# Performance work log

Measured on AMD Instinct MI355X. Metric: run time of the kernel, lower is better.

## Reference

```python
import jax, jax.numpy as jnp
import numpy as np

T, B, H, OUT = 64, 4096, 256, 2
SLOPE = 25.0  # snntorch surrogate.fast_sigmoid default slope


@jax.custom_vjp
def spike(x):
    # Heaviside forward, fast-sigmoid surrogate gradient backward
    return (x > 0).astype(x.dtype)

def _spk_fwd(x):
    return (x > 0).astype(x.dtype), x

def _spk_bwd(x, g):
    return (g / (SLOPE * jnp.abs(x) + 1.0) ** 2,)

spike.defvjp(_spk_fwd, _spk_bwd)


def temporal_embedding(length):
    center = length // 2
    sigma = length / 10
    pos = np.arange(length)
    e = np.exp(-0.5 * ((pos - center) / sigma) ** 2)
    e = (e - e.min()) / (e.max() - e.min())
    return jnp.asarray(e, dtype=jnp.float32)


def setup_inputs() -> dict:
    key = jax.random.key(0)
    ks = jax.random.split(key, 16)

    def lin(k, o, i):
        bound = 1.0 / np.sqrt(i)
        kw, kb = jax.random.split(k)
        W = jax.random.uniform(kw, (o, i), minval=-bound, maxval=bound, dtype=jnp.float32)
        b = jax.random.uniform(kb, (o,), minval=-bound, maxval=bound, dtype=jnp.float32)
        return W, b

    W_in, b_in = lin(ks[0], H, 3)
    W_h, b_h = lin(ks[1], H, H)
    W_h2, b_h2 = lin(ks[2], H, H)
    W_out, b_out = lin(ks[3], OUT, H)
    W_pred, b_pred = lin(ks[4], OUT, T * 4)
    u = lambda k, n: jax.random.uniform(k, (n,), dtype=jnp.float32)
    return {
        "x": jax.random.normal(ks[5], (T, B, 3), dtype=jnp.float32),
        "W_in": W_in, "b_in": b_in,
        "beta_in": u(ks[6], H), "thr_in": u(ks[7], H),
        "W_h": W_h, "b_h": b_h,
        "beta_h": u(ks[8], H), "thr_h": u(ks[9], H),
        "W_h2": W_h2, "b_h2": b_h2,
        "beta_h2": u(ks[10], H), "thr_h2": u(ks[11], H),
        "W_out": W_out, "b_out": b_out,
        "beta_out": u(ks[12], OUT),
        "W_pred": W_pred, "b_pred": b_pred,
    }


def reference(x, W_in, b_in, beta_in, thr_in, W_h, b_h, beta_h, thr_h,
              W_h2, b_h2, beta_h2, thr_h2, W_out, b_out, beta_out,
              W_pred, b_pred):
    Tn, Bsz = x.shape[0], x.shape[1]
    emb = temporal_embedding(Tn)
    x = x * emb[:, None, None]  # per-timestep Gaussian temporal weighting

    def lif(cur, mem, beta, thr):
        # snnTorch Leaky, reset_mechanism='subtract': reset from PREVIOUS mem (detached)
        reset = jax.lax.stop_gradient((mem - thr > 0).astype(cur.dtype))
        mem = jnp.clip(beta, 0.0, 1.0) * mem + cur - reset * thr
        return spike(mem - thr), mem

    def step(carry, x_t):
        m1, m2, m4, m3 = carry
        s1, m1 = lif(x_t @ W_in.T + b_in, m1, beta_in, thr_in)
        s2, m2 = lif(s1 @ W_h.T + b_h, m2, beta_h, thr_h)
        s4, m4 = lif(s2 @ W_h2.T + b_h2, m4, beta_h2, thr_h2)
        # li_out: reset_mechanism='none', default threshold=1.0
        m3 = jnp.clip(beta_out, 0.0, 1.0) * m3 + s4 @ W_out.T + b_out
        spk_out = spike(m3 - 1.0)
        return (m1, m2, m4, m3), (spk_out, m3)

    z = lambda n: jnp.zeros((Bsz, n), x.dtype)
    init = (z(W_in.shape[0]), z(W_h.shape[0]), z(W_h2.shape[0]), z(W_out.shape[0]))
    _, (spk_rec, mem_rec) = jax.lax.scan(step, init, x)
    out = jnp.concatenate([spk_rec, mem_rec], axis=-1)  # [T, B, 2*OUT]
    # torch .view(B, T*2*OUT) on contiguous [T,B,2*OUT] == plain reshape
    out = out.reshape(Bsz, Tn * out.shape[-1])
    return out @ W_pred.T + b_pred  # [B, OUT]
```

## Files before the change

kernel.cpp:

```cpp
#include <hip/hip_runtime.h>
#include <hip/hip_bf16.h>

#define TT 64
#define BB 4096
#define HH 256
#define BMb 16
#define NBLK (BB / BMb)
#define TC 4
#define NCH (TT / TC)

typedef short bf16x8_t __attribute__((ext_vector_type(8)));
typedef float f32x4_t  __attribute__((ext_vector_type(4)));

#define WS_WA_B   0u
#define WS_EMB_B  786432u
#define WS_REC_B  1048576u

__device__ __forceinline__ float clip01f(float v) {
    return fminf(fmaxf(v, 0.0f), 1.0f);
}

__global__ __launch_bounds__(64) void setup_emb_kernel(float* __restrict__ emb) {
    int i = threadIdx.x;
    const double sigma = 64.0 / 10.0;
    const double c = 32.0;
    double d = ((double)i - c) / sigma;
    double e = exp(-0.5 * (d * d));
    double d0 = (0.0 - c) / sigma;
    double emin = exp(-0.5 * (d0 * d0));
    emb[i] = (float)((e - emin) / (1.0 - emin));
}

__global__ __launch_bounds__(256) void split_weights_kernel(
    const float* __restrict__ W_h, const float* __restrict__ W_h2,
    unsigned short* __restrict__ WA)
{
    int flat = blockIdx.x * 256 + threadIdx.x;
    int j     = flat & 7;
    int lane  = (flat >> 3) & 63;
    int ntile = (flat >> 9) & 15;
    int kt    = (flat >> 13) & 7;
    int rest  = flat >> 16;
    int part  = rest % 3;
    int layer = rest / 3;
    int k = kt * 32 + (lane >> 4) * 8 + j;
    int n = ntile * 16 + (lane & 15);
    const float* W = layer ? W_h2 : W_h;
    float w = W[n * HH + k];
    __hip_bfloat16 h = __float2bfloat16(w);
    float r1 = w - __bfloat162float(h);
    __hip_bfloat16 m = __float2bfloat16(r1);
    float r2 = r1 - __bfloat162float(m);
    __hip_bfloat16 l = __float2bfloat16(r2);
    __hip_bfloat16 v = (part == 0) ? h : ((part == 1) ? m : l);
    WA[flat] = *reinterpret_cast<unsigned short*>(&v);
}

union U16x8 { uint4 u; bf16x8_t v; };


#define AS1 __attribute__((address_space(1)))
#define AS3 __attribute__((address_space(3)))
__device__ __forceinline__ void gl16(const void* g, void* l) {
    __builtin_amdgcn_global_load_lds((AS1 const void*)g, (AS3 void*)l, 16, 0, 0);
}

#define ISSUE6(Wc, ktn, sl) do {                                               \
    const char* gb_ = (const char*)(Wc) + (ktn) * 16384;                       \
    char* lb_ = myring + (sl) * 6144;                                          \
    gl16(gb_,          lb_);                                                   \
    gl16(gb_ + 1024,   lb_ + 1024);                                            \
    gl16(gb_ + 131072, lb_ + 2048);                                            \
    gl16(gb_ + 132096, lb_ + 3072);                                            \
    gl16(gb_ + 262144, lb_ + 4096);                                            \
    gl16(gb_ + 263168, lb_ + 5120);                                            \
} while (0)

#define MFMA8T(wa_, wb_, ktb) do {                                             \
    _Pragma("unroll")                                                          \
    for (int tt_ = 0; tt_ < TC; ++tt_) {                                       \
        U16x8 br_; br_.u = BfL[tt_ * 512 + (ktb) * 64];                        \
        D0[tt_] = __builtin_amdgcn_mfma_f32_16x16x32_bf16(wa_.v, br_.v, D0[tt_], 0, 0, 0); \
        D1[tt_] = __builtin_amdgcn_mfma_f32_16x16x32_bf16(wb_.v, br_.v, D1[tt_], 0, 0, 0); \
    }                                                                          \
} while (0)

#define STEPT(sl, ktb, Wi, kti) do {                                           \
    asm volatile("s_waitcnt vmcnt(6)" ::: "memory");                           \
    __builtin_amdgcn_sched_barrier(0);                                         \
    {                                                                          \
        U16x8 wa_, wb_;                                                        \
        wa_.u = ringRd[(sl) * 384 + 0];                                        \
        wb_.u = ringRd[(sl) * 384 + 64];                                       \
        asm volatile("s_waitcnt lgkmcnt(0)" ::: "memory");                     \
        __builtin_amdgcn_sched_barrier(0);                                     \
        MFMA8T(wa_, wb_, ktb);                                                 \
    }                                                                          \
    {                                                                          \
        U16x8 wa_, wb_;                                                        \
        wa_.u = ringRd[(sl) * 384 + 128];                                      \
        wb_.u = ringRd[(sl) * 384 + 192];                                      \
        asm volatile("s_waitcnt lgkmcnt(0)" ::: "memory");                     \
        __builtin_amdgcn_sched_barrier(0);                                     \
        MFMA8T(wa_, wb_, ktb);                                                 \
    }                                                                          \
    {                                                                          \
        U16x8 wa_, wb_;                                                        \
        wa_.u = ringRd[(sl) * 384 + 256];                                      \
        wb_.u = ringRd[(sl) * 384 + 320];                                      \
        asm volatile("s_waitcnt lgkmcnt(0)" ::: "memory");                     \
        __builtin_amdgcn_sched_barrier(0);                                     \
        ISSUE6(Wi, kti, sl);                                                   \
        __builtin_amdgcn_sched_barrier(0);                                     \
        MFMA8T(wa_, wb_, ktb);                                                 \
    }                                                                          \
} while (0)

#define GPHASE(Wc, Wn) do {                                                    \
    STEPT(0, 0, Wc, 2);                                                        \
    STEPT(1, 1, Wc, 3);                                                        \
    STEPT(0, 2, Wc, 4);                                                        \
    STEPT(1, 3, Wc, 5);                                                        \
    STEPT(0, 4, Wc, 6);                                                        \
    STEPT(1, 5, Wc, 7);                                                        \
    STEPT(0, 6, Wn, 0);                                                        \
    STEPT(1, 7, Wn, 1);                                                        \
} while (0)

__device__ __forceinline__ void compute_p(
    const float* __restrict__ WoutS, const unsigned long long (*__restrict__ M3Lt)[4],
    int wb, int ooc, float* __restrict__ pout, int lane)
{
    if (lane < 32) {
        float p = 0.f;
        for (int k = 0; k < HH; ++k) {
            int ww = k >> 4, gg = (k >> 2) & 3, reg = k & 3;
            unsigned long long word = M3Lt[ww][reg];
            unsigned w32 = (gg < 2) ? (unsigned)word : (unsigned)(word >> 32);
            int sh = ((gg & 1) << 4) | wb;
            unsigned bit = (w32 >> sh) & 1u;
            float wv = WoutS[ooc * HH + k];
            p = p + (bit ? wv : 0.f);
        }
        pout[lane] = p;
    }
}

__device__ __forceinline__ void li_walker_bits(
    const float* __restrict__ WoutS, const unsigned long long (*__restrict__ M3Lt)[4],
    int wb, int ooc, float bto, float bo, float& m3s,
    float* __restrict__ rec, int t, int b0, int lane)
{
    if (lane < 32) {
        float p = 0.f;
        for (int k = 0; k < HH; ++k) {
            int ww = k >> 4, gg = (k >> 2) & 3, reg = k & 3;
            unsigned long long word = M3Lt[ww][reg];
            unsigned w32 = (gg < 2) ? (unsigned)word : (unsigned)(word >> 32);
            int sh = ((gg & 1) << 4) | wb;
            unsigned bit = (w32 >> sh) & 1u;
            float wv = WoutS[ooc * HH + k];
            p = p + (bit ? wv : 0.f);
        }
        float mm3 = fmaf(bto, m3s, p);
        mm3 = mm3 + bo;
        m3s = mm3;
        float spk = ((m3s - 1.0f) > 0.f) ? 1.f : 0.f;
        float om3 = __shfl_xor(m3s, 16, 64);
        float osp = __shfl_xor(spk, 16, 64);
        if (lane < 16) {
            *(float4*)(rec + ((size_t)t * BB + b0 + wb) * 4) =
                make_float4(spk, osp, m3s, om3);
        }
    }
}

__global__ __launch_bounds__(512) void snn_main_kernel(
    const float* __restrict__ x,
    const float* __restrict__ W_in, const float* __restrict__ b_in,
    const float* __restrict__ beta_in, const float* __restrict__ thr_in,
    const float* __restrict__ b_h, const float* __restrict__ beta_h, const float* __restrict__ thr_h,
    const float* __restrict__ b_h2, const float* __restrict__ beta_h2, const float* __restrict__ thr_h2,
    const float* __restrict__ W_out, const float* __restrict__ b_out, const float* __restrict__ beta_out,
    const unsigned short* __restrict__ WA, const float* __restrict__ emb,
    float* __restrict__ rec)
{
#pragma clang fp contract(off)
    const int tid = threadIdx.x;
    const int w = tid >> 6;
    const int lane = tid & 63;
    const int b = lane & 15;
    const int g = lane >> 4;
    const int b0 = blockIdx.x * BMb;

    __shared__ __align__(16) unsigned short frag[TC][8 * 64 * 8];
    __shared__ unsigned long long M3L[TC][16][4];
    __shared__ float pbuf[TC][32];
    __shared__ __align__(16) float WoutS[2 * HH];
    __shared__ float4 PL1a[HH];
    __shared__ float2 PL1b[HH];
    __shared__ float4 PL2[HH];
    __shared__ float4 PL3[HH];
    __shared__ float  xs[TT][BMb][3];
    __shared__ float  embS[TT];
    __shared__ __align__(16) char ring[8 * 2 * 6144];

    char* myring = ring + w * 12288;
    const uint4* ringRd = (const uint4*)(ring + w * 12288 + lane * 16);
    const uint4* BfL = (const uint4*)frag + lane;

    WoutS[tid] = W_out[tid];
    if (tid < HH) {
        int n = tid;
        PL1a[n] = make_float4(W_in[n * 3], W_in[n * 3 + 1], W_in[n * 3 + 2], b_in[n]);
        PL1b[n] = make_float2(clip01f(beta_in[n]), thr_in[n]);
        PL2[n]  = make_float4(b_h[n],  clip01f(beta_h[n]),  thr_h[n],  0.f);
        PL3[n]  = make_float4(b_h2[n], clip01f(beta_h2[n]), thr_h2[n], 0.f);
    }
    if (tid < TT) embS[tid] = emb[tid];
#pragma unroll
    for (int i = tid; i < TT * BMb; i += 512) {
        int ts = i >> 4, bb = i & 15;
        const float* xp = x + ((size_t)ts * BB + b0 + bb) * 3;
        xs[ts][bb][0] = xp[0];
        xs[ts][bb][1] = xp[1];
        xs[ts][bb][2] = xp[2];
    }

    const int nb0 = w * 32 + g * 4;

    float m1[2][4], m2[2][4], m4[2][4];
#pragma unroll
    for (int u = 0; u < 2; ++u)
#pragma unroll
        for (int r = 0; r < 4; ++r) { m1[u][r] = 0.f; m2[u][r] = 0.f; m4[u][r] = 0.f; }

    const int sb0 = ((w * 64 + ((g >> 1) * 16 + b)) * 8 + (g & 1) * 4);

    const int wb = lane & 15;
    const int ooc = (lane >> 4) & 1;
    float bto = clip01f(beta_out[ooc]);
    float bo = b_out[ooc];
    float m3s = 0.f;

    const uint4* W2 = (const uint4*)WA + (size_t)(2 * w) * 64 + lane;
    const uint4* W3 = W2 + 24576;

    ISSUE6(W2, 0, 0);
    ISSUE6(W2, 1, 1);

    __syncthreads();

#pragma unroll 1
    for (int c = 0; c < NCH; ++c) {
        const int t0 = c * TC;

#pragma unroll
        for (int tt = 0; tt < TC; ++tt) {
            const int t = t0 + tt;
            float et = embS[t];
            float xe0 = xs[t][b][0] * et;
            float xe1 = xs[t][b][1] * et;
            float xe2 = xs[t][b][2] * et;
            unsigned sp[2][4];
#pragma unroll
            for (int u = 0; u < 2; ++u)
#pragma unroll
            for (int r = 0; r < 4; ++r) {
                int n = nb0 + u * 16 + r;
                float4 pa = PL1a[n];
                float2 pb = PL1b[n];
                float a1 = xe0 * pa.x;
                a1 = fmaf(xe1, pa.y, a1);
                a1 = fmaf(xe2, pa.z, a1);
                float cur = a1 + pa.w;
                float rf = ((m1[u][r] - pb.y) > 0.f) ? 1.f : 0.f;
                float mm = fmaf(pb.x, m1[u][r], cur);
                mm = fmaf(-rf, pb.y, mm);
                m1[u][r] = mm;
                sp[u][r] = ((mm - pb.y) > 0.f) ? 0x3F80u : 0u;
            }
            *(uint2*)(&frag[tt][sb0])       = make_uint2(sp[0][0] | (sp[0][1] << 16), sp[0][2] | (sp[0][3] << 16));
            *(uint2*)(&frag[tt][sb0 + 256]) = make_uint2(sp[1][0] | (sp[1][1] << 16), sp[1][2] | (sp[1][3] << 16));
        }
        __syncthreads();

        if (w < TC && c > 0)
            compute_p(WoutS, M3L[w], wb, ooc, pbuf[w], lane);

        f32x4_t D0[TC], D1[TC];
#pragma unroll
        for (int tt = 0; tt < TC; ++tt) {
            D0[tt] = (f32x4_t){0.f, 0.f, 0.f, 0.f};
            D1[tt] = (f32x4_t){0.f, 0.f, 0.f, 0.f};
        }
        GPHASE(W2, W3);

        uint2 s2w[TC][2];
#pragma unroll
        for (int tt = 0; tt < TC; ++tt) {
            unsigned sp[2][4];
#pragma unroll
            for (int r = 0; r < 4; ++r) {
                int n0 = nb0 + r;
                float4 p2 = PL2[n0];
                float cur = D0[tt][r] + p2.x;
                float rf = ((m2[0][r] - p2.z) > 0.f) ? 1.f : 0.f;
                float mm = fmaf(p2.y, m2[0][r], cur);
                mm = fmaf(-rf, p2.z, mm);
                m2[0][r] = mm;
                sp[0][r] = ((mm - p2.z) > 0.f) ? 0x3F80u : 0u;
            }
#pragma unroll
            for (int r = 0; r < 4; ++r) {
                int n1 = nb0 + 16 + r;
                float4 p2 = PL2[n1];
                float cur = D1[tt][r] + p2.x;
                float rf = ((m2[1][r] - p2.z) > 0.f) ? 1.f : 0.f;
                float mm = fmaf(p2.y, m2[1][r], cur);
                mm = fmaf(-rf, p2.z, mm);
                m2[1][r] = mm;
                sp[1][r] = ((mm - p2.z) > 0.f) ? 0x3F80u : 0u;
            }
            s2w[tt][0] = make_uint2(sp[0][0] | (sp[0][1] << 16), sp[0][2] | (sp[0][3] << 16));
            s2w[tt][1] = make_uint2(sp[1][0] | (sp[1][1] << 16), sp[1][2] | (sp[1][3] << 16));
        }
        __syncthreads();

        if (w == 0 && c > 0 && lane < 32) {
#pragma unroll
            for (int tt = 0; tt < TC; ++tt) {
                float p = pbuf[tt][lane];
                float mm3 = fmaf(bto, m3s, p);
                mm3 = mm3 + bo;
                m3s = mm3;
                float spk = ((m3s - 1.0f) > 0.f) ? 1.f : 0.f;
                float om3 = __shfl_xor(m3s, 16, 64);
                float osp = __shfl_xor(spk, 16, 64);
                if (lane < 16) {
                    *(float4*)(rec + ((size_t)(t0 - TC + tt) * BB + b0 + wb) * 4) =
                        make_float4(spk, osp, m3s, om3);
                }
            }
        }

#pragma unroll
        for (int tt = 0; tt < TC; ++tt) {
            *(uint2*)(&frag[tt][sb0])       = s2w[tt][0];
            *(uint2*)(&frag[tt][sb0 + 256]) = s2w[tt][1];
        }
        __syncthreads();

#pragma unroll
        for (int tt = 0; tt < TC; ++tt) {
            D0[tt] = (f32x4_t){0.f, 0.f, 0.f, 0.f};
            D1[tt] = (f32x4_t){0.f, 0.f, 0.f, 0.f};
        }
        GPHASE(W3, W2);

#pragma unroll
        for (int tt = 0; tt < TC; ++tt) {
#pragma unroll
            for (int u = 0; u < 2; ++u) {
#pragma unroll
                for (int r = 0; r < 4; ++r) {
                    int n = nb0 + u * 16 + r;
                    float4 p3 = PL3[n];
                    float cur = ((u == 0) ? D0[tt][r] : D1[tt][r]) + p3.x;
                    float rf = ((m4[u][r] - p3.z) > 0.f) ? 1.f : 0.f;
                    float mm = fmaf(p3.y, m4[u][r], cur);
                    mm = fmaf(-rf, p3.z, mm);
                    m4[u][r] = mm;
                    bool s3 = (mm - p3.z) > 0.f;
                    unsigned long long mk = __ballot(s3);
                    if (lane == 0) M3L[tt][2 * w + u][r] = mk;
                }
            }
        }
        __syncthreads();
    }

    if (w == 0) {
#pragma unroll
        for (int tt = 0; tt < TC; ++tt)
            li_walker_bits(WoutS, M3L[tt], wb, ooc, bto, bo, m3s,
                           rec, TT - TC + tt, b0, lane);
    }
}

__global__ __launch_bounds__(256) void pred_kernel(
    const float* __restrict__ rec, const float* __restrict__ W_pred,
    const float* __restrict__ b_pred, float* __restrict__ out)
{
#pragma clang fp contract(off)
    int r = blockIdx.x * 256 + threadIdx.x;
    const float* f = rec + (size_t)r * 256;
    float a0 = 0.f, a1 = 0.f;
#pragma unroll 4
    for (int c = 0; c < 256; ++c) {
        float v = f[c];
        a0 = fmaf(v, W_pred[c], a0);
        a1 = fmaf(v, W_pred[256 + c], a1);
    }
    out[r * 2 + 0] = a0 + b_pred[0];
    out[r * 2 + 1] = a1 + b_pred[1];
}

extern "C" void kernel_launch(void* const* d_in, const int* in_sizes, int n_in,
                              void* d_out, int out_size, void* d_ws, size_t ws_size,
                              hipStream_t stream)
{
    const float* x        = (const float*)d_in[0];
    const float* W_in     = (const float*)d_in[1];
    const float* b_in     = (const float*)d_in[2];
    const float* beta_in  = (const float*)d_in[3];
    const float* thr_in   = (const float*)d_in[4];
    const float* W_h      = (const float*)d_in[5];
    const float* b_h      = (const float*)d_in[6];
    const float* beta_h   = (const float*)d_in[7];
    const float* thr_h    = (const float*)d_in[8];
    const float* W_h2     = (const float*)d_in[9];
    const float* b_h2     = (const float*)d_in[10];
    const float* beta_h2  = (const float*)d_in[11];
    const float* thr_h2   = (const float*)d_in[12];
    const float* W_out    = (const float*)d_in[13];
    const float* b_out    = (const float*)d_in[14];
    const float* beta_out = (const float*)d_in[15];
    const float* W_pred   = (const float*)d_in[16];
    const float* b_pred   = (const float*)d_in[17];

    char* ws = (char*)d_ws;
    unsigned short* WA = (unsigned short*)(ws + WS_WA_B);
    float* emb = (float*)(ws + WS_EMB_B);
    float* rec = (float*)(ws + WS_REC_B);

    split_weights_kernel<<<1536, 256, 0, stream>>>(W_h, W_h2, WA);
    setup_emb_kernel<<<1, 64, 0, stream>>>(emb);

    snn_main_kernel<<<NBLK, 512, 0, stream>>>(
        x, W_in, b_in, beta_in, thr_in,
        b_h, beta_h, thr_h,
        b_h2, beta_h2, thr_h2,
        W_out, b_out, beta_out,
        WA, emb, rec);

    pred_kernel<<<BB / 256, 256, 0, stream>>>(rec, W_pred, b_pred, (float*)d_out);
}
```

Before: 668.3 us.

## Halve main kernel to 4 waves each computing 64 output neurons

The main SNN kernel now runs 256 threads (4 waves) instead of 512. Each wave owns 64 hidden neurons instead of 32, so every B fragment loaded from LDS feeds four MFMAs instead of two, and the per-wave weight ring doubles to 12 async loads per stage. The aim is fewer waves contending for LDS and barriers, with more reuse of the spike fragments per wave. The cost is higher register pressure (16 accumulators per timestep chunk, larger membrane arrays) and less latency hiding per block, which may lower occupancy.

```diff
diff --git a/kernel.cpp b/kernel.cpp
--- a/kernel.cpp
+++ b/kernel.cpp
@@ -65,54 +65,68 @@
     __builtin_amdgcn_global_load_lds((AS1 const void*)g, (AS3 void*)l, 16, 0, 0);
 }
 
-#define ISSUE6(Wc, ktn, sl) do {                                               \
+#define ISSUE12(Wc, ktn, sl) do {                                              \
     const char* gb_ = (const char*)(Wc) + (ktn) * 16384;                       \
-    char* lb_ = myring + (sl) * 6144;                                          \
-    gl16(gb_,          lb_);                                                   \
-    gl16(gb_ + 1024,   lb_ + 1024);                                            \
-    gl16(gb_ + 131072, lb_ + 2048);                                            \
-    gl16(gb_ + 132096, lb_ + 3072);                                            \
-    gl16(gb_ + 262144, lb_ + 4096);                                            \
-    gl16(gb_ + 263168, lb_ + 5120);                                            \
+    char* lb_ = myring + (sl) * 12288;                                         \
+    gl16(gb_,            lb_);                                                 \
+    gl16(gb_ + 1024,     lb_ + 1024);                                          \
+    gl16(gb_ + 2048,     lb_ + 2048);                                          \
+    gl16(gb_ + 3072,     lb_ + 3072);                                          \
+    gl16(gb_ + 131072,   lb_ + 4096);                                          \
+    gl16(gb_ + 132096,   lb_ + 5120);                                          \
+    gl16(gb_ + 133120,   lb_ + 6144);                                          \
+    gl16(gb_ + 134144,   lb_ + 7168);                                          \
+    gl16(gb_ + 262144,   lb_ + 8192);                                          \
+    gl16(gb_ + 263168,   lb_ + 9216);                                          \
+    gl16(gb_ + 264192,   lb_ + 10240);                                         \
+    gl16(gb_ + 265216,   lb_ + 11264);                                         \
 } while (0)
 
-#define MFMA8T(wa_, wb_, ktb) do {                                             \
+#define MFMA16(ktb) do {                                                       \
     _Pragma("unroll")                                                          \
     for (int tt_ = 0; tt_ < TC; ++tt_) {                                       \
         U16x8 br_; br_.u = BfL[tt_ * 512 + (ktb) * 64];                        \
-        D0[tt_] = __builtin_amdgcn_mfma_f32_16x16x32_bf16(wa_.v, br_.v, D0[tt_], 0, 0, 0); \
-        D1[tt_] = __builtin_amdgcn_mfma_f32_16x16x32_bf16(wb_.v, br_.v, D1[tt_], 0, 0, 0); \
+        D[tt_][0] = __builtin_amdgcn_mfma_f32_16x16x32_bf16(w0_.v, br_.v, D[tt_][0], 0, 0, 0); \
+        D[tt_][1] = __builtin_amdgcn_mfma_f32_16x16x32_bf16(w1_.v, br_.v, D[tt_][1], 0, 0, 0); \
+        D[tt_][2] = __builtin_amdgcn_mfma_f32_16x16x32_bf16(w2_.v, br_.v, D[tt_][2], 0, 0, 0); \
+        D[tt_][3] = __builtin_amdgcn_mfma_f32_16x16x32_bf16(w3_.v, br_.v, D[tt_][3], 0, 0, 0); \
     }                                                                          \
 } while (0)
 
 #define STEPT(sl, ktb, Wi, kti) do {                                           \
-    asm volatile("s_waitcnt vmcnt(6)" ::: "memory");                           \
+    asm volatile("s_waitcnt vmcnt(12)" ::: "memory");                          \
     __builtin_amdgcn_sched_barrier(0);                                         \
     {                                                                          \
-        U16x8 wa_, wb_;                                                        \
-        wa_.u = ringRd[(sl) * 384 + 0];                                        \
-        wb_.u = ringRd[(sl) * 384 + 64];                                       \
+        U16x8 w0_, w1_, w2_, w3_;                                              \
+        w0_.u = ringRd[(sl) * 768 + 0];                                        \
+        w1_.u = ringRd[(sl) * 768 + 64];                                       \
+        w2_.u = ringRd[(sl) * 768 + 128];                                      \
+        w3_.u = ringRd[(sl) * 768 + 192];                                      \
         asm volatile("s_waitcnt lgkmcnt(0)" ::: "memory");                     \
         __builtin_amdgcn_sched_barrier(0);                                     \
-        MFMA8T(wa_, wb_, ktb);                                                 \
+        MFMA16(ktb);                                                           \
     }                                                                          \
     {                                                                          \
-        U16x8 wa_, wb_;                                                        \
-        wa_.u = ringRd[(sl) * 384 + 128];                                      \
-        wb_.u = ringRd[(sl) * 384 + 192];                                      \
+        U16x8 w0_, w1_, w2_, w3_;                                              \
+        w0_.u = ringRd[(sl) * 768 + 256];                                      \
+        w1_.u = ringRd[(sl) * 768 + 320];                                      \
+        w2_.u = ringRd[(sl) * 768 + 384];                                      \
+        w3_.u = ringRd[(sl) * 768 + 448];                                      \
         asm volatile("s_waitcnt lgkmcnt(0)" ::: "memory");                     \
         __builtin_amdgcn_sched_barrier(0);                                     \
-        MFMA8T(wa_, wb_, ktb);                                                 \
+        MFMA16(ktb);                                                           \
     }                                                                          \
     {                                                                          \
-        U16x8 wa_, wb_;                                                        \
-        wa_.u = ringRd[(sl) * 384 + 256];                                      \
-        wb_.u = ringRd[(sl) * 384 + 320];                                      \
+        U16x8 w0_, w1_, w2_, w3_;                                              \
+        w0_.u = ringRd[(sl) * 768 + 512];                                      \
+        w1_.u = ringRd[(sl) * 768 + 576];                                      \
+        w2_.u = ringRd[(sl) * 768 + 640];                                      \
+        w3_.u = ringRd[(sl) * 768 + 704];                                      \
         asm volatile("s_waitcnt lgkmcnt(0)" ::: "memory");                     \
         __builtin_amdgcn_sched_barrier(0);                                     \
-        ISSUE6(Wi, kti, sl);                                                   \
+        ISSUE12(Wi, kti, sl);                                                  \
         __builtin_amdgcn_sched_barrier(0);                                     \
-        MFMA8T(wa_, wb_, ktb);                                                 \
+        MFMA16(ktb);                                                           \
     }                                                                          \
 } while (0)
 
@@ -175,7 +189,7 @@
     }
 }
 
-__global__ __launch_bounds__(512) void snn_main_kernel(
+__global__ __launch_bounds__(256) void snn_main_kernel(
     const float* __restrict__ x,
     const float* __restrict__ W_in, const float* __restrict__ b_in,
     const float* __restrict__ beta_in, const float* __restrict__ thr_in,
@@ -203,14 +217,15 @@
     __shared__ float4 PL3[HH];
     __shared__ float  xs[TT][BMb][3];
     __shared__ float  embS[TT];
-    __shared__ __align__(16) char ring[8 * 2 * 6144];
-
-    char* myring = ring + w * 12288;
-    const uint4* ringRd = (const uint4*)(ring + w * 12288 + lane * 16);
+    __shared__ __align__(16) char ring[4 * 2 * 12288];
+
+    char* myring = ring + w * 24576;
+    const uint4* ringRd = (const uint4*)(ring + w * 24576 + lane * 16);
     const uint4* BfL = (const uint4*)frag + lane;
 
-    WoutS[tid] = W_out[tid];
-    if (tid < HH) {
+#pragma unroll
+    for (int i = tid; i < 2 * HH; i += 256) WoutS[i] = W_out[i];
+    {
         int n = tid;
         PL1a[n] = make_float4(W_in[n * 3], W_in[n * 3 + 1], W_in[n * 3 + 2], b_in[n]);
         PL1b[n] = make_float2(clip01f(beta_in[n]), thr_in[n]);
@@ -219,7 +234,7 @@
     }
     if (tid < TT) embS[tid] = emb[tid];
 #pragma unroll
-    for (int i = tid; i < TT * BMb; i += 512) {
+    for (int i = tid; i < TT * BMb; i += 256) {
         int ts = i >> 4, bb = i & 15;
         const float* xp = x + ((size_t)ts * BB + b0 + bb) * 3;
         xs[ts][bb][0] = xp[0];
@@ -227,15 +242,15 @@
         xs[ts][bb][2] = xp[2];
     }
 
-    const int nb0 = w * 32 + g * 4;
-
-    float m1[2][4], m2[2][4], m4[2][4];
-#pragma unroll
-    for (int u = 0; u < 2; ++u)
+    const int nb0 = w * 64 + g * 4;
+
+    float m1[4][4], m2[4][4], m4[4][4];
+#pragma unroll
+    for (int u = 0; u < 4; ++u)
 #pragma unroll
         for (int r = 0; r < 4; ++r) { m1[u][r] = 0.f; m2[u][r] = 0.f; m4[u][r] = 0.f; }
 
-    const int sb0 = ((w * 64 + ((g >> 1) * 16 + b)) * 8 + (g & 1) * 4);
+    const int sbB = ((2 * w) * 64 + ((g >> 1) * 16 + b)) * 8 + (g & 1) * 4;
 
     const int wb = lane & 15;
     const int ooc = (lane >> 4) & 1;
@@ -243,11 +258,11 @@
     float bo = b_out[ooc];
     float m3s = 0.f;
 
-    const uint4* W2 = (const uint4*)WA + (size_t)(2 * w) * 64 + lane;
+    const uint4* W2 = (const uint4*)WA + (size_t)(4 * w) * 64 + lane;
     const uint4* W3 = W2 + 24576;
 
-    ISSUE6(W2, 0, 0);
-    ISSUE6(W2, 1, 1);
+    ISSUE12(W2, 0, 0);
+    ISSUE12(W2, 1, 1);
 
     __syncthreads();
 
@@ -262,9 +277,9 @@
             float xe0 = xs[t][b][0] * et;
             float xe1 = xs[t][b][1] * et;
             float xe2 = xs[t][b][2] * et;
-            unsigned sp[2][4];
-#pragma unroll
-            for (int u = 0; u < 2; ++u)
+            unsigned sp[4][4];
+#pragma unroll
+            for (int u = 0; u < 4; ++u)
 #pragma unroll
             for (int r = 0; r < 4; ++r) {
                 int n = nb0 + u * 16 + r;
@@ -280,50 +295,43 @@
                 m1[u][r] = mm;
                 sp[u][r] = ((mm - pb.y) > 0.f) ? 0x3F80u : 0u;
             }
-            *(uint2*)(&frag[tt][sb0])       = make_uint2(sp[0][0] | (sp[0][1] << 16), sp[0][2] | (sp[0][3] << 16));
-            *(uint2*)(&frag[tt][sb0 + 256]) = make_uint2(sp[1][0] | (sp[1][1] << 16), sp[1][2] | (sp[1][3] << 16));
+            *(uint2*)(&frag[tt][sbB])       = make_uint2(sp[0][0] | (sp[0][1] << 16), sp[0][2] | (sp[0][3] << 16));
+            *(uint2*)(&frag[tt][sbB + 256]) = make_uint2(sp[1][0] | (sp[1][1] << 16), sp[1][2] | (sp[1][3] << 16));
+            *(uint2*)(&frag[tt][sbB + 512]) = make_uint2(sp[2][0] | (sp[2][1] << 16), sp[2][2] | (sp[2][3] << 16));
+            *(uint2*)(&frag[tt][sbB + 768]) = make_uint2(sp[3][0] | (sp[3][1] << 16), sp[3][2] | (sp[3][3] << 16));
         }
         __syncthreads();
 
-        if (w < TC && c > 0)
+        if (c > 0)
             compute_p(WoutS, M3L[w], wb, ooc, pbuf[w], lane);
 
-        f32x4_t D0[TC], D1[TC];
+        f32x4_t D[TC][4];
+#pragma unroll
+        for (int tt = 0; tt < TC; ++tt)
+#pragma unroll
+            for (int u = 0; u < 4; ++u)
+                D[tt][u] = (f32x4_t){0.f, 0.f, 0.f, 0.f};
+        GPHASE(W2, W3);
+
+        uint2 s2w[TC][4];
 #pragma unroll
         for (int tt = 0; tt < TC; ++tt) {
-            D0[tt] = (f32x4_t){0.f, 0.f, 0.f, 0.f};
-            D1[tt] = (f32x4_t){0.f, 0.f, 0.f, 0.f};
-        }
-        GPHASE(W2, W3);
-
-        uint2 s2w[TC][2];
-#pragma unroll
-        for (int tt = 0; tt < TC; ++tt) {
-            unsigned sp[2][4];
-#pragma unroll
-            for (int r = 0; r < 4; ++r) {
-                int n0 = nb0 + r;
-                float4 p2 = PL2[n0];
-                float cur = D0[tt][r] + p2.x;
-                float rf = ((m2[0][r] - p2.z) > 0.f) ? 1.f : 0.f;
-                float mm = fmaf(p2.y, m2[0][r], cur);
-                mm = fmaf(-rf, p2.z, mm);
-                m2[0][r] = mm;
-                sp[0][r] = ((mm - p2.z) > 0.f) ? 0x3F80u : 0u;
+#pragma unroll
+            for (int u = 0; u < 4; ++u) {
+                unsigned sp[4];
+#pragma unroll
+                for (int r = 0; r < 4; ++r) {
+                    int n = nb0 + u * 16 + r;
+                    float4 p2 = PL2[n];
+                    float cur = D[tt][u][r] + p2.x;
+                    float rf = ((m2[u][r] - p2.z) > 0.f) ? 1.f : 0.f;
+                    float mm = fmaf(p2.y, m2[u][r], cur);
+                    mm = fmaf(-rf, p2.z, mm);
+                    m2[u][r] = mm;
+                    sp[r] = ((mm - p2.z) > 0.f) ? 0x3F80u : 0u;
+                }
+                s2w[tt][u] = make_uint2(sp[0] | (sp[1] << 16), sp[2] | (sp[3] << 16));
             }
-#pragma unroll
-            for (int r = 0; r < 4; ++r) {
-                int n1 = nb0 + 16 + r;
-                float4 p2 = PL2[n1];
-                float cur = D1[tt][r] + p2.x;
-                float rf = ((m2[1][r] - p2.z) > 0.f) ? 1.f : 0.f;
-                float mm = fmaf(p2.y, m2[1][r], cur);
-                mm = fmaf(-rf, p2.z, mm);
-                m2[1][r] = mm;
-                sp[1][r] = ((mm - p2.z) > 0.f) ? 0x3F80u : 0u;
-            }
-            s2w[tt][0] = make_uint2(sp[0][0] | (sp[0][1] << 16), sp[0][2] | (sp[0][3] << 16));
-            s2w[tt][1] = make_uint2(sp[1][0] | (sp[1][1] << 16), sp[1][2] | (sp[1][3] << 16));
         }
         __syncthreads();
 
@@ -346,34 +354,36 @@
 
 #pragma unroll
         for (int tt = 0; tt < TC; ++tt) {
-            *(uint2*)(&frag[tt][sb0])       = s2w[tt][0];
-            *(uint2*)(&frag[tt][sb0 + 256]) = s2w[tt][1];
+            *(uint2*)(&frag[tt][sbB])       = s2w[tt][0];
+            *(uint2*)(&frag[tt][sbB + 256]) = s2w[tt][1];
+            *(uint2*)(&frag[tt][sbB + 512]) = s2w[tt][2];
+            *(uint2*)(&frag[tt][sbB + 768]) = s2w[tt][3];
         }
         __syncthreads();
 
 #pragma unroll
+        for (int tt = 0; tt < TC; ++tt)
+#pragma unroll
+            for (int u = 0; u < 4; ++u)
+                D[tt][u] = (f32x4_t){0.f, 0.f, 0.f, 0.f};
+        GPHASE(W3, W2);
+
+#pragma unroll
         for (int tt = 0; tt < TC; ++tt) {
-            D0[tt] = (f32x4_t){0.f, 0.f, 0.f, 0.f};
-            D1[tt] = (f32x4_t){0.f, 0.f, 0.f, 0.f};
-        }
-        GPHASE(W3, W2);
-
-#pragma unroll
-        for (int tt = 0; tt < TC; ++tt) {
-#pragma unroll
-            for (int u = 0; u < 2; ++u) {
+#pragma unroll
+            for (int u = 0; u < 4; ++u) {
 #pragma unroll
                 for (int r = 0; r < 4; ++r) {
                     int n = nb0 + u * 16 + r;
                     float4 p3 = PL3[n];
-                    float cur = ((u == 0) ? D0[tt][r] : D1[tt][r]) + p3.x;
+                    float cur = D[tt][u][r] + p3.x;
                     float rf = ((m4[u][r] - p3.z) > 0.f) ? 1.f : 0.f;
                     float mm = fmaf(p3.y, m4[u][r], cur);
                     mm = fmaf(-rf, p3.z, mm);
                     m4[u][r] = mm;
                     bool s3 = (mm - p3.z) > 0.f;
                     unsigned long long mk = __ballot(s3);
-                    if (lane == 0) M3L[tt][2 * w + u][r] = mk;
+                    if (lane == 0) M3L[tt][4 * w + u][r] = mk;
                 }
             }
         }
@@ -437,7 +447,7 @@
     split_weights_kernel<<<1536, 256, 0, stream>>>(W_h, W_h2, WA);
     setup_emb_kernel<<<1, 64, 0, stream>>>(emb);
 
-    snn_main_kernel<<<NBLK, 512, 0, stream>>>(
+    snn_main_kernel<<<NBLK, 256, 0, stream>>>(
         x, W_in, b_in, beta_in, thr_in,
         b_h, beta_h, thr_h,
         b_h2, beta_h2, thr_h2,
```

Result: slower. 1.018 ms (+52.4%).
